# Performance work log

Hardware: AMD Instinct MI355X
Metric: run time of the kernel (lower is better)

The kernel has to match this reference:

```python
import jax, jax.numpy as jnp
import numpy as np

D = 384      # n_embed_dims
H = 6        # n_heads
HS = D // H  # head_size = 64
T = 256      # block_size
B = 256
EPS = 1e-5


def setup_inputs() -> dict:
    key = jax.random.key(0)
    ks = jax.random.split(key, 12)
    s_in = 1.0 / np.sqrt(D)
    s_ff = 1.0 / np.sqrt(4 * D)
    return {
        "x": jax.random.normal(ks[0], (B, T, D), jnp.float32),
        # per-head QKV weights, stacked [H, D, HS] (Linear bias=False)
        "wq": jax.random.normal(ks[1], (H, D, HS), jnp.float32) * s_in,
        "wk": jax.random.normal(ks[2], (H, D, HS), jnp.float32) * s_in,
        "wv": jax.random.normal(ks[3], (H, D, HS), jnp.float32) * s_in,
        "w_proj": jax.random.normal(ks[4], (D, D), jnp.float32) * s_in,
        "b_proj": jax.random.normal(ks[5], (D,), jnp.float32) * s_in,
        "w1": jax.random.normal(ks[6], (D, 4 * D), jnp.float32) * s_in,
        "b1": jax.random.normal(ks[7], (4 * D,), jnp.float32) * s_in,
        "w2": jax.random.normal(ks[8], (4 * D, D), jnp.float32) * s_ff,
        "b2": jax.random.normal(ks[9], (D,), jnp.float32) * s_ff,
        "g1": jnp.ones((D,), jnp.float32),
        "be1": jnp.zeros((D,), jnp.float32),
        "g2": jnp.ones((D,), jnp.float32),
        "be2": jnp.zeros((D,), jnp.float32),
    }


def _layernorm(x, g, b):
    mu = jnp.mean(x, axis=-1, keepdims=True)
    var = jnp.mean(jnp.square(x - mu), axis=-1, keepdims=True)
    return (x - mu) * jax.lax.rsqrt(var + EPS) * g + b


def _attention(x, wq, wk, wv, w_proj, b_proj):
    # faithful quirk: scale = 1/sqrt(C) with C = full embed dim (384)
    scale = 1.0 / jnp.sqrt(jnp.asarray(D, x.dtype))
    q = jnp.einsum("btd,hde->bhte", x, wq)  # [B,H,T,HS]
    k = jnp.einsum("btd,hde->bhte", x, wk)
    v = jnp.einsum("btd,hde->bhte", x, wv)
    w = jnp.einsum("bhte,bhse->bhts", q, k) * scale  # [B,H,T,T], no mask
    w = jax.nn.softmax(w, axis=-1)
    out = jnp.einsum("bhts,bhse->bhte", w, v)  # [B,H,T,HS]
    # concat heads along feature dim (head order matches torch cat)
    out = out.transpose(0, 2, 1, 3).reshape(x.shape[0], x.shape[1], D)
    return out @ w_proj + b_proj


def reference(x, wq, wk, wv, w_proj, b_proj, w1, b1, w2, b2, g1, be1, g2, be2):
    x = x + _attention(_layernorm(x, g1, be1), wq, wk, wv, w_proj, b_proj)
    h = _layernorm(x, g2, be2)
    h = jax.nn.relu(h @ w1 + b1) @ w2 + b2  # dropout = eval-mode identity
    return x + h
```

## Files before the change

### kernel.cpp

```cpp
#include <hip/hip_runtime.h>
#include <stdint.h>

#define NTOK 65536
#define DE 384
#define S_HEAD 25165824

typedef __bf16 bf16x8 __attribute__((ext_vector_type(8)));
typedef float  f32x4 __attribute__((ext_vector_type(4)));

__device__ __forceinline__ unsigned short f2bf(float f) {
  union { float fl; unsigned u; } a; a.fl = f;
  unsigned r = a.u + 0x7fffu + ((a.u >> 16) & 1u);
  return (unsigned short)(r >> 16);
}

__device__ __forceinline__ void gll16(const void* g, void* l) {
  __builtin_amdgcn_global_load_lds((const __attribute__((address_space(1))) void*)g,
                                   (__attribute__((address_space(3))) void*)l, 16, 0, 0);
}

__device__ __forceinline__ bf16x8 ds128(unsigned addr) {
  bf16x8 r;
  asm volatile("ds_read_b128 %0, %1" : "=v"(r) : "v"(addr));
  return r;
}

__global__ void pack_t(unsigned short* __restrict__ dst, const float* __restrict__ src,
                       int R, int C) {
  int t = blockIdx.x * 256 + threadIdx.x;
  if (t >= R * C) return;
  int r = t / C, c = t - r * C;
  dst[(size_t)c * R + r] = f2bf(src[t]);
}

__global__ void qkv_pack(const float* __restrict__ wq, const float* __restrict__ wk,
                         const float* __restrict__ wv, unsigned short* __restrict__ dst) {
  int t = blockIdx.x * 256 + threadIdx.x;
  if (t >= 3 * 147456) return;
  int which = t / 147456, r = t - which * 147456;
  const float* src = which == 0 ? wq : (which == 1 ? wk : wv);
  int h = r / 24576, r2 = r - h * 24576;
  int d = r2 >> 6, e = r2 & 63;
  dst[(size_t)(which * 384 + h * 64 + e) * 384 + d] = f2bf(src[r]);
}

__global__ __launch_bounds__(256) void ln_kernel(const float* __restrict__ x,
                                                 const float* __restrict__ g,
                                                 const float* __restrict__ be,
                                                 unsigned short* __restrict__ out) {
  int wave = threadIdx.x >> 6, lane = threadIdx.x & 63;
  size_t row = (size_t)blockIdx.x * 4 + wave;
  const float* xr = x + row * DE;
  int c0 = lane * 2;
  float2 v0 = *(const float2*)(xr + c0);
  float2 v1 = *(const float2*)(xr + 128 + c0);
  float2 v2 = *(const float2*)(xr + 256 + c0);
  float s  = v0.x + v0.y + v1.x + v1.y + v2.x + v2.y;
  float ss = v0.x*v0.x + v0.y*v0.y + v1.x*v1.x + v1.y*v1.y + v2.x*v2.x + v2.y*v2.y;
#pragma unroll
  for (int m = 1; m < 64; m <<= 1) { s += __shfl_xor(s, m); ss += __shfl_xor(ss, m); }
  float mu = s * (1.0f / 384.0f);
  float rstd = rsqrtf(ss * (1.0f / 384.0f) - mu * mu + 1e-5f);
  unsigned short* orow = out + row * DE;
  {
    float a0 = (v0.x - mu) * rstd * g[c0] + be[c0];
    float a1 = (v0.y - mu) * rstd * g[c0 + 1] + be[c0 + 1];
    *(unsigned*)(orow + c0) = (unsigned)f2bf(a0) | ((unsigned)f2bf(a1) << 16);
  }
  {
    int c = c0 + 128;
    float a0 = (v1.x - mu) * rstd * g[c] + be[c];
    float a1 = (v1.y - mu) * rstd * g[c + 1] + be[c + 1];
    *(unsigned*)(orow + c) = (unsigned)f2bf(a0) | ((unsigned)f2bf(a1) << 16);
  }
  {
    int c = c0 + 256;
    float a0 = (v2.x - mu) * rstd * g[c] + be[c];
    float a1 = (v2.y - mu) * rstd * g[c + 1] + be[c + 1];
    *(unsigned*)(orow + c) = (unsigned)f2bf(a0) | ((unsigned)f2bf(a1) << 16);
  }
}

template<int EPI>
__device__ __forceinline__
void gemm_core(const unsigned short* __restrict__ A, const unsigned short* __restrict__ Bt,
               int M, int N, int K, int ntx,
               const float* __restrict__ bias, const float* __restrict__ resid,
               float* __restrict__ outf, unsigned short* __restrict__ outb) {
  __shared__ __align__(16) unsigned short As[2][8192];
  __shared__ __align__(16) unsigned short Bs[2][8192];
  const int tid = threadIdx.x;
  const int wave = tid >> 6, lane = tid & 63;

  const int nwg = gridDim.x;
  const int cpx = nwg >> 3;
  const int wg = (blockIdx.x & 7) * cpx + (blockIdx.x >> 3);
  const int bx = wg % ntx, by = wg / ntx;
  const int mBase = by << 7, nBase = bx << 7;
  const int wm = (wave >> 1) << 6, wn = (wave & 1) << 6;
  const int fr = lane & 15, fg = lane >> 4;

  const unsigned asb = (unsigned)(uintptr_t)&As[0][0];
  const unsigned bsb = (unsigned)(uintptr_t)&Bs[0][0];

  f32x4 acc[4][4];
  const f32x4 z = {0.f, 0.f, 0.f, 0.f};
#pragma unroll
  for (int i = 0; i < 4; ++i)
#pragma unroll
    for (int j = 0; j < 4; ++j) acc[i][j] = z;

  auto stage = [&](int buf, int kt) {
#pragma unroll
    for (int i = 0; i < 4; ++i) {
      int Lb = i * 4096 + wave * 1024;
      int L = Lb + lane * 16;
      int row = L >> 7;
      int col = (((L >> 4) & 7) ^ (row & 7)) << 3;
      gll16(A + (size_t)(mBase + row) * K + kt + col, (unsigned short*)As[buf] + (Lb >> 1));
    }
#pragma unroll
    for (int i = 0; i < 4; ++i) {
      int Lb = i * 4096 + wave * 1024;
      int L = Lb + lane * 16;
      int row = L >> 7;
      int col = (((L >> 4) & 7) ^ (row & 7)) << 3;
      gll16(Bt + (size_t)(nBase + row) * K + kt + col, (unsigned short*)Bs[buf] + (Lb >> 1));
    }
  };

  const int NK = K >> 6;
  stage(0, 0);
  for (int t = 0; t < NK; ++t) {
    const int cur = t & 1;
    if (t + 1 < NK) {
      stage(cur ^ 1, (t + 1) << 6);
      asm volatile("s_waitcnt vmcnt(8)" ::: "memory");
    } else {
      asm volatile("s_waitcnt vmcnt(0)" ::: "memory");
    }
    asm volatile("" ::: "memory");
    __builtin_amdgcn_s_barrier();
    asm volatile("" ::: "memory");

    const unsigned ab = asb + (cur ? 16384u : 0u);
    const unsigned bb = bsb + (cur ? 16384u : 0u);
    bf16x8 af[2][4], bfr[2][4];
#pragma unroll
    for (int ks = 0; ks < 2; ++ks) {
#pragma unroll
      for (int mb = 0; mb < 4; ++mb) {
        int row = wm + mb * 16 + fr;
        unsigned byte = (unsigned)(row << 7) + ((unsigned)((ks * 4 + fg) ^ (row & 7)) << 4);
        af[ks][mb] = ds128(ab + byte);
      }
#pragma unroll
      for (int nb = 0; nb < 4; ++nb) {
        int row = wn + nb * 16 + fr;
        unsigned byte = (unsigned)(row << 7) + ((unsigned)((ks * 4 + fg) ^ (row & 7)) << 4);
        bfr[ks][nb] = ds128(bb + byte);
      }
    }
    asm volatile("s_waitcnt lgkmcnt(0)" ::: "memory");
    __builtin_amdgcn_sched_barrier(0);
    __builtin_amdgcn_s_setprio(1);
#pragma unroll
    for (int ks = 0; ks < 2; ++ks)
#pragma unroll
      for (int mb = 0; mb < 4; ++mb)
#pragma unroll
        for (int nb = 0; nb < 4; ++nb)
          acc[mb][nb] = __builtin_amdgcn_mfma_f32_16x16x32_bf16(af[ks][mb], bfr[ks][nb], acc[mb][nb], 0, 0, 0);
    __builtin_amdgcn_s_setprio(0);
    asm volatile("" ::: "memory");
    __builtin_amdgcn_s_barrier();
    asm volatile("" ::: "memory");
  }

#pragma unroll
  for (int mb = 0; mb < 4; ++mb) {
#pragma unroll
    for (int nb = 0; nb < 4; ++nb) {
      const int gn = nBase + wn + nb * 16 + fr;
#pragma unroll
      for (int i = 0; i < 4; ++i) {
        const int gm = mBase + wm + mb * 16 + (fg << 2) + i;
        float val = acc[mb][nb][i];
        if (EPI == 0) {
          int which = gn / 384;
          int rest = gn - which * 384;
          int hh = rest >> 6, e = rest & 63;
          int b = gm >> 8, tt = gm & 255;
          size_t idx;
          if (which < 2)
            idx = (size_t)which * S_HEAD + (((size_t)(b * 6 + hh) * 256 + tt) << 6) + e;
          else
            idx = 2 * (size_t)S_HEAD + (((size_t)(b * 6 + hh) * 64 + e) << 8) + tt;
          outb[idx] = f2bf(val);
        } else if (EPI == 1) {
          size_t idx = (size_t)gm * N + gn;
          outf[idx] = val + bias[gn] + resid[idx];
        } else if (EPI == 2) {
          float r = val + bias[gn];
          outb[(size_t)gm * N + gn] = f2bf(r > 0.f ? r : 0.f);
        } else {
          size_t idx = (size_t)gm * N + gn;
          outf[idx] = val + bias[gn] + resid[idx];
        }
      }
    }
  }
}

__global__ __launch_bounds__(256, 2)
void gemm_qkv(const unsigned short* __restrict__ A, const unsigned short* __restrict__ Bt,
              int M, int N, int K, int ntx, const float* __restrict__ bias,
              const float* __restrict__ resid, float* __restrict__ outf,
              unsigned short* __restrict__ outb) {
  gemm_core<0>(A, Bt, M, N, K, ntx, bias, resid, outf, outb);
}
__global__ __launch_bounds__(256, 2)
void gemm_proj(const unsigned short* __restrict__ A, const unsigned short* __restrict__ Bt,
               int M, int N, int K, int ntx, const float* __restrict__ bias,
               const float* __restrict__ resid, float* __restrict__ outf,
               unsigned short* __restrict__ outb) {
  gemm_core<1>(A, Bt, M, N, K, ntx, bias, resid, outf, outb);
}
__global__ __launch_bounds__(256, 2)
void gemm_mlp1(const unsigned short* __restrict__ A, const unsigned short* __restrict__ Bt,
               int M, int N, int K, int ntx, const float* __restrict__ bias,
               const float* __restrict__ resid, float* __restrict__ outf,
               unsigned short* __restrict__ outb) {
  gemm_core<2>(A, Bt, M, N, K, ntx, bias, resid, outf, outb);
}
__global__ __launch_bounds__(256, 2)
void gemm_mlp2(const unsigned short* __restrict__ A, const unsigned short* __restrict__ Bt,
               int M, int N, int K, int ntx, const float* __restrict__ bias,
               const float* __restrict__ resid, float* __restrict__ outf,
               unsigned short* __restrict__ outb) {
  gemm_core<3>(A, Bt, M, N, K, ntx, bias, resid, outf, outb);
}

__global__ __launch_bounds__(256)
void attn_kernel(const unsigned short* __restrict__ q, const unsigned short* __restrict__ kk,
                 const unsigned short* __restrict__ vt, unsigned short* __restrict__ o) {
  __shared__ unsigned short Pw[4][64 * 32];
  const int bh = blockIdx.x;
  const int b = bh / 6, h = bh - b * 6;
  const unsigned short* qb = q + (size_t)bh * 256 * 64;
  const unsigned short* kb = kk + (size_t)bh * 256 * 64;
  const unsigned short* vb = vt + (size_t)bh * 64 * 256;
  const int wave = threadIdx.x >> 6, lane = threadIdx.x & 63;
  const int fr = lane & 15, fg = lane >> 4;
  const int fk = fg << 3;
  const int qrow0 = wave << 6;
  const float scale = 0.051031036307982884f;
  const f32x4 z = {0.f, 0.f, 0.f, 0.f};

  bf16x8 qf[4][2];
#pragma unroll
  for (int rb = 0; rb < 4; ++rb)
#pragma unroll
    for (int ks = 0; ks < 2; ++ks)
      qf[rb][ks] = *(const bf16x8*)(qb + (qrow0 + rb * 16 + fr) * 64 + ks * 32 + fk);

  float pm[4][4];
#pragma unroll
  for (int rb = 0; rb < 4; ++rb)
#pragma unroll
    for (int i = 0; i < 4; ++i) pm[rb][i] = -1e30f;

  for (int cb = 0; cb < 16; ++cb) {
    bf16x8 kf0 = *(const bf16x8*)(kb + (cb * 16 + fr) * 64 + fk);
    bf16x8 kf1 = *(const bf16x8*)(kb + (cb * 16 + fr) * 64 + 32 + fk);
#pragma unroll
    for (int rb = 0; rb < 4; ++rb) {
      f32x4 s = __builtin_amdgcn_mfma_f32_16x16x32_bf16(qf[rb][0], kf0, z, 0, 0, 0);
      s = __builtin_amdgcn_mfma_f32_16x16x32_bf16(qf[rb][1], kf1, s, 0, 0, 0);
#pragma unroll
      for (int i = 0; i < 4; ++i) pm[rb][i] = fmaxf(pm[rb][i], s[i]);
    }
  }
#pragma unroll
  for (int rb = 0; rb < 4; ++rb)
#pragma unroll
    for (int i = 0; i < 4; ++i) {
      float v = pm[rb][i];
      v = fmaxf(v, __shfl_xor(v, 1));
      v = fmaxf(v, __shfl_xor(v, 2));
      v = fmaxf(v, __shfl_xor(v, 4));
      v = fmaxf(v, __shfl_xor(v, 8));
      pm[rb][i] = v;
    }

  f32x4 oacc[4][4];
  float psum[4][4];
#pragma unroll
  for (int rb = 0; rb < 4; ++rb)
#pragma unroll
    for (int nb = 0; nb < 4; ++nb) oacc[rb][nb] = z;
#pragma unroll
  for (int rb = 0; rb < 4; ++rb)
#pragma unroll
    for (int i = 0; i < 4; ++i) psum[rb][i] = 0.f;

  for (int kb2 = 0; kb2 < 8; ++kb2) {
#pragma unroll
    for (int c2 = 0; c2 < 2; ++c2) {
      int cb = kb2 * 2 + c2;
      bf16x8 kf0 = *(const bf16x8*)(kb + (cb * 16 + fr) * 64 + fk);
      bf16x8 kf1 = *(const bf16x8*)(kb + (cb * 16 + fr) * 64 + 32 + fk);
#pragma unroll
      for (int rb = 0; rb < 4; ++rb) {
        f32x4 s = __builtin_amdgcn_mfma_f32_16x16x32_bf16(qf[rb][0], kf0, z, 0, 0, 0);
        s = __builtin_amdgcn_mfma_f32_16x16x32_bf16(qf[rb][1], kf1, s, 0, 0, 0);
#pragma unroll
        for (int i = 0; i < 4; ++i) {
          float p = __expf(scale * (s[i] - pm[rb][i]));
          psum[rb][i] += p;
          Pw[wave][(rb * 16 + (fg << 2) + i) * 32 + c2 * 16 + fr] = f2bf(p);
        }
      }
    }
    bf16x8 pa[4], vf[4];
#pragma unroll
    for (int rb = 0; rb < 4; ++rb) pa[rb] = *(const bf16x8*)(&Pw[wave][(rb * 16 + fr) * 32 + fk]);
#pragma unroll
    for (int nb = 0; nb < 4; ++nb)
      vf[nb] = *(const bf16x8*)(vb + (nb * 16 + fr) * 256 + kb2 * 32 + fk);
#pragma unroll
    for (int rb = 0; rb < 4; ++rb)
#pragma unroll
      for (int nb = 0; nb < 4; ++nb)
        oacc[rb][nb] = __builtin_amdgcn_mfma_f32_16x16x32_bf16(pa[rb], vf[nb], oacc[rb][nb], 0, 0, 0);
  }

  float rs[4][4];
#pragma unroll
  for (int rb = 0; rb < 4; ++rb)
#pragma unroll
    for (int i = 0; i < 4; ++i) {
      float v = psum[rb][i];
      v += __shfl_xor(v, 1);
      v += __shfl_xor(v, 2);
      v += __shfl_xor(v, 4);
      v += __shfl_xor(v, 8);
      rs[rb][i] = 1.0f / v;
    }

#pragma unroll
  for (int rb = 0; rb < 4; ++rb)
#pragma unroll
    for (int nb = 0; nb < 4; ++nb)
#pragma unroll
      for (int i = 0; i < 4; ++i) {
        int token = b * 256 + qrow0 + rb * 16 + (fg << 2) + i;
        int gcol = h * 64 + nb * 16 + fr;
        o[(size_t)token * DE + gcol] = f2bf(oacc[rb][nb][i] * rs[rb][i]);
      }
}

extern "C" void kernel_launch(void* const* d_in, const int* in_sizes, int n_in,
                              void* d_out, int out_size, void* d_ws, size_t ws_size,
                              hipStream_t stream) {
  const float* x     = (const float*)d_in[0];
  const float* wq    = (const float*)d_in[1];
  const float* wk    = (const float*)d_in[2];
  const float* wv    = (const float*)d_in[3];
  const float* wproj = (const float*)d_in[4];
  const float* bproj = (const float*)d_in[5];
  const float* w1    = (const float*)d_in[6];
  const float* b1    = (const float*)d_in[7];
  const float* w2    = (const float*)d_in[8];
  const float* b2    = (const float*)d_in[9];
  const float* g1    = (const float*)d_in[10];
  const float* be1   = (const float*)d_in[11];
  const float* g2    = (const float*)d_in[12];
  const float* be2   = (const float*)d_in[13];

  char* ws = (char*)d_ws;
  unsigned short* xln   = (unsigned short*)(ws + 0);
  unsigned short* hbuf  = xln;
  unsigned short* qkv   = (unsigned short*)(ws + 50331648);
  unsigned short* attno = (unsigned short*)(ws + 201326592);
  unsigned short* act   = (unsigned short*)(ws + 50331648);
  float*          x1    = (float*)(ws + 251658240);
  unsigned short* wqkvt = (unsigned short*)(ws + 352321536);
  unsigned short* wprjt = (unsigned short*)(ws + 352321536 + 884736);
  unsigned short* w1t   = (unsigned short*)(ws + 352321536 + 884736 + 294912);
  unsigned short* w2t   = (unsigned short*)(ws + 352321536 + 884736 + 294912 + 1179648);

  qkv_pack<<<(3 * 147456 + 255) / 256, 256, 0, stream>>>(wq, wk, wv, wqkvt);
  pack_t<<<(147456 + 255) / 256, 256, 0, stream>>>(wprjt, wproj, 384, 384);
  pack_t<<<(589824 + 255) / 256, 256, 0, stream>>>(w1t, w1, 384, 1536);
  pack_t<<<(589824 + 255) / 256, 256, 0, stream>>>(w2t, w2, 1536, 384);

  ln_kernel<<<NTOK / 4, 256, 0, stream>>>(x, g1, be1, xln);

  gemm_qkv<<<512 * 9, 256, 0, stream>>>(xln, wqkvt, NTOK, 1152, 384, 9,
                                        nullptr, nullptr, nullptr, qkv);

  attn_kernel<<<1536, 256, 0, stream>>>(qkv, qkv + S_HEAD, qkv + 2 * (size_t)S_HEAD, attno);

  gemm_proj<<<512 * 3, 256, 0, stream>>>(attno, wprjt, NTOK, 384, 384, 3,
                                         bproj, x, x1, nullptr);

  ln_kernel<<<NTOK / 4, 256, 0, stream>>>(x1, g2, be2, hbuf);

  gemm_mlp1<<<512 * 12, 256, 0, stream>>>(hbuf, w1t, NTOK, 1536, 384, 12,
                                          b1, nullptr, nullptr, act);

  gemm_mlp2<<<512 * 3, 256, 0, stream>>>(act, w2t, NTOK, 384, 1536, 3,
                                         b2, x1, (float*)d_out, nullptr);
}
```

Baseline: 584.0 us.

## Use 256-wide GEMM tiles with 8 waves and row-major QKV output

Generalizes the GEMM core to templated block and wave tiling and moves all GEMMs to 256x256 or 256x128 tiles with 512 threads, loading A fragments in halves to limit register pressure. The QKV weight matrix is padded to 1280 columns so the QKV GEMM writes a plain row-major [tokens,1280] buffer instead of scattering per-head and transposed V. The attention kernel now reads Q/K with the wider stride and transposes V into swizzled shared memory itself. The intent is more operand reuse per tile and coalesced epilogue stores, at the cost of padding work, an extra LDS transpose in attention, and lower occupancy.

```diff
diff --git a/kernel.cpp b/kernel.cpp
--- a/kernel.cpp
+++ b/kernel.cpp
@@ -3,10 +3,11 @@
 
 #define NTOK 65536
 #define DE 384
-#define S_HEAD 25165824
+#define QSTR 1280
 
 typedef __bf16 bf16x8 __attribute__((ext_vector_type(8)));
 typedef float  f32x4 __attribute__((ext_vector_type(4)));
+typedef unsigned short u16x8 __attribute__((ext_vector_type(8)));
 
 __device__ __forceinline__ unsigned short f2bf(float f) {
   union { float fl; unsigned u; } a; a.fl = f;
@@ -36,12 +37,16 @@
 __global__ void qkv_pack(const float* __restrict__ wq, const float* __restrict__ wk,
                          const float* __restrict__ wv, unsigned short* __restrict__ dst) {
   int t = blockIdx.x * 256 + threadIdx.x;
-  if (t >= 3 * 147456) return;
-  int which = t / 147456, r = t - which * 147456;
-  const float* src = which == 0 ? wq : (which == 1 ? wk : wv);
-  int h = r / 24576, r2 = r - h * 24576;
-  int d = r2 >> 6, e = r2 & 63;
-  dst[(size_t)(which * 384 + h * 64 + e) * 384 + d] = f2bf(src[r]);
+  if (t >= QSTR * 384) return;
+  int n = t / 384, k = t - n * 384;
+  unsigned short v = 0;
+  if (n < 1152) {
+    int which = n / 384, r = n - which * 384;
+    const float* src = which == 0 ? wq : (which == 1 ? wk : wv);
+    int h = r >> 6, e = r & 63;
+    v = f2bf(src[h * 24576 + k * 64 + e]);
+  }
+  dst[t] = v;
 }
 
 __global__ __launch_bounds__(256) void ln_kernel(const float* __restrict__ x,
@@ -81,14 +86,20 @@
   }
 }
 
-template<int EPI>
+template<int EPI, int BM, int BN, int WM, int WN>
 __device__ __forceinline__
 void gemm_core(const unsigned short* __restrict__ A, const unsigned short* __restrict__ Bt,
                int M, int N, int K, int ntx,
                const float* __restrict__ bias, const float* __restrict__ resid,
                float* __restrict__ outf, unsigned short* __restrict__ outb) {
-  __shared__ __align__(16) unsigned short As[2][8192];
-  __shared__ __align__(16) unsigned short Bs[2][8192];
+  constexpr int T = WM * WN * 64;
+  constexpr int MWT = BM / WM, NWT = BN / WN;
+  constexpr int MF = MWT / 16, NF = NWT / 16;
+  constexpr int MH = MF / 4;
+  constexpr int LA = (BM * 128) / (T * 16);
+  constexpr int LB = (BN * 128) / (T * 16);
+  __shared__ __align__(16) unsigned short As[2][BM * 64];
+  __shared__ __align__(16) unsigned short Bs[2][BN * 64];
   const int tid = threadIdx.x;
   const int wave = tid >> 6, lane = tid & 63;
 
@@ -96,32 +107,33 @@
   const int cpx = nwg >> 3;
   const int wg = (blockIdx.x & 7) * cpx + (blockIdx.x >> 3);
   const int bx = wg % ntx, by = wg / ntx;
-  const int mBase = by << 7, nBase = bx << 7;
-  const int wm = (wave >> 1) << 6, wn = (wave & 1) << 6;
+  const int mBase = by * BM, nBase = bx * BN;
+  const int wmi = wave / WN, wni = wave % WN;
+  const int wm = wmi * MWT, wn = wni * NWT;
   const int fr = lane & 15, fg = lane >> 4;
 
   const unsigned asb = (unsigned)(uintptr_t)&As[0][0];
   const unsigned bsb = (unsigned)(uintptr_t)&Bs[0][0];
 
-  f32x4 acc[4][4];
+  f32x4 acc[MF][NF];
   const f32x4 z = {0.f, 0.f, 0.f, 0.f};
 #pragma unroll
-  for (int i = 0; i < 4; ++i)
-#pragma unroll
-    for (int j = 0; j < 4; ++j) acc[i][j] = z;
+  for (int i = 0; i < MF; ++i)
+#pragma unroll
+    for (int j = 0; j < NF; ++j) acc[i][j] = z;
 
   auto stage = [&](int buf, int kt) {
 #pragma unroll
-    for (int i = 0; i < 4; ++i) {
-      int Lb = i * 4096 + wave * 1024;
+    for (int i = 0; i < LA; ++i) {
+      int Lb = i * (T * 16) + wave * 1024;
       int L = Lb + lane * 16;
       int row = L >> 7;
       int col = (((L >> 4) & 7) ^ (row & 7)) << 3;
       gll16(A + (size_t)(mBase + row) * K + kt + col, (unsigned short*)As[buf] + (Lb >> 1));
     }
 #pragma unroll
-    for (int i = 0; i < 4; ++i) {
-      int Lb = i * 4096 + wave * 1024;
+    for (int i = 0; i < LB; ++i) {
+      int Lb = i * (T * 16) + wave * 1024;
       int L = Lb + lane * 16;
       int row = L >> 7;
       int col = (((L >> 4) & 7) ^ (row & 7)) << 3;
@@ -135,7 +147,8 @@
     const int cur = t & 1;
     if (t + 1 < NK) {
       stage(cur ^ 1, (t + 1) << 6);
-      asm volatile("s_waitcnt vmcnt(8)" ::: "memory");
+      if constexpr (LA + LB == 8) asm volatile("s_waitcnt vmcnt(8)" ::: "memory");
+      else                        asm volatile("s_waitcnt vmcnt(6)" ::: "memory");
     } else {
       asm volatile("s_waitcnt vmcnt(0)" ::: "memory");
     }
@@ -143,60 +156,54 @@
     __builtin_amdgcn_s_barrier();
     asm volatile("" ::: "memory");
 
-    const unsigned ab = asb + (cur ? 16384u : 0u);
-    const unsigned bb = bsb + (cur ? 16384u : 0u);
-    bf16x8 af[2][4], bfr[2][4];
+    const unsigned ab = asb + (cur ? (unsigned)(BM * 128) : 0u);
+    const unsigned bb = bsb + (cur ? (unsigned)(BN * 128) : 0u);
 #pragma unroll
     for (int ks = 0; ks < 2; ++ks) {
-#pragma unroll
-      for (int mb = 0; mb < 4; ++mb) {
-        int row = wm + mb * 16 + fr;
-        unsigned byte = (unsigned)(row << 7) + ((unsigned)((ks * 4 + fg) ^ (row & 7)) << 4);
-        af[ks][mb] = ds128(ab + byte);
-      }
-#pragma unroll
-      for (int nb = 0; nb < 4; ++nb) {
+      bf16x8 bfr[NF];
+#pragma unroll
+      for (int nb = 0; nb < NF; ++nb) {
         int row = wn + nb * 16 + fr;
         unsigned byte = (unsigned)(row << 7) + ((unsigned)((ks * 4 + fg) ^ (row & 7)) << 4);
-        bfr[ks][nb] = ds128(bb + byte);
+        bfr[nb] = ds128(bb + byte);
       }
-    }
-    asm volatile("s_waitcnt lgkmcnt(0)" ::: "memory");
-    __builtin_amdgcn_sched_barrier(0);
-    __builtin_amdgcn_s_setprio(1);
-#pragma unroll
-    for (int ks = 0; ks < 2; ++ks)
-#pragma unroll
-      for (int mb = 0; mb < 4; ++mb)
-#pragma unroll
-        for (int nb = 0; nb < 4; ++nb)
-          acc[mb][nb] = __builtin_amdgcn_mfma_f32_16x16x32_bf16(af[ks][mb], bfr[ks][nb], acc[mb][nb], 0, 0, 0);
-    __builtin_amdgcn_s_setprio(0);
+#pragma unroll
+      for (int mh = 0; mh < MH; ++mh) {
+        bf16x8 af[4];
+#pragma unroll
+        for (int mb = 0; mb < 4; ++mb) {
+          int row = wm + (mh * 4 + mb) * 16 + fr;
+          unsigned byte = (unsigned)(row << 7) + ((unsigned)((ks * 4 + fg) ^ (row & 7)) << 4);
+          af[mb] = ds128(ab + byte);
+        }
+        asm volatile("s_waitcnt lgkmcnt(0)" ::: "memory");
+        __builtin_amdgcn_sched_barrier(0);
+        __builtin_amdgcn_s_setprio(1);
+#pragma unroll
+        for (int mb = 0; mb < 4; ++mb)
+#pragma unroll
+          for (int nb = 0; nb < NF; ++nb)
+            acc[mh * 4 + mb][nb] =
+                __builtin_amdgcn_mfma_f32_16x16x32_bf16(af[mb], bfr[nb], acc[mh * 4 + mb][nb], 0, 0, 0);
+        __builtin_amdgcn_s_setprio(0);
+      }
+    }
     asm volatile("" ::: "memory");
     __builtin_amdgcn_s_barrier();
     asm volatile("" ::: "memory");
   }
 
 #pragma unroll
-  for (int mb = 0; mb < 4; ++mb) {
-#pragma unroll
-    for (int nb = 0; nb < 4; ++nb) {
+  for (int mb = 0; mb < MF; ++mb) {
+#pragma unroll
+    for (int nb = 0; nb < NF; ++nb) {
       const int gn = nBase + wn + nb * 16 + fr;
 #pragma unroll
       for (int i = 0; i < 4; ++i) {
         const int gm = mBase + wm + mb * 16 + (fg << 2) + i;
         float val = acc[mb][nb][i];
         if (EPI == 0) {
-          int which = gn / 384;
-          int rest = gn - which * 384;
-          int hh = rest >> 6, e = rest & 63;
-          int b = gm >> 8, tt = gm & 255;
-          size_t idx;
-          if (which < 2)
-            idx = (size_t)which * S_HEAD + (((size_t)(b * 6 + hh) * 256 + tt) << 6) + e;
-          else
-            idx = 2 * (size_t)S_HEAD + (((size_t)(b * 6 + hh) * 64 + e) << 8) + tt;
-          outb[idx] = f2bf(val);
+          outb[(size_t)gm * N + gn] = f2bf(val);
         } else if (EPI == 1) {
           size_t idx = (size_t)gm * N + gn;
           outf[idx] = val + bias[gn] + resid[idx];
@@ -212,44 +219,45 @@
   }
 }
 
-__global__ __launch_bounds__(256, 2)
+__global__ __launch_bounds__(512, 1)
 void gemm_qkv(const unsigned short* __restrict__ A, const unsigned short* __restrict__ Bt,
               int M, int N, int K, int ntx, const float* __restrict__ bias,
               const float* __restrict__ resid, float* __restrict__ outf,
               unsigned short* __restrict__ outb) {
-  gemm_core<0>(A, Bt, M, N, K, ntx, bias, resid, outf, outb);
-}
-__global__ __launch_bounds__(256, 2)
+  gemm_core<0, 256, 256, 2, 4>(A, Bt, M, N, K, ntx, bias, resid, outf, outb);
+}
+__global__ __launch_bounds__(512, 1)
 void gemm_proj(const unsigned short* __restrict__ A, const unsigned short* __restrict__ Bt,
                int M, int N, int K, int ntx, const float* __restrict__ bias,
                const float* __restrict__ resid, float* __restrict__ outf,
                unsigned short* __restrict__ outb) {
-  gemm_core<1>(A, Bt, M, N, K, ntx, bias, resid, outf, outb);
-}
-__global__ __launch_bounds__(256, 2)
+  gemm_core<1, 256, 128, 4, 2>(A, Bt, M, N, K, ntx, bias, resid, outf, outb);
+}
+__global__ __launch_bounds__(512, 1)
 void gemm_mlp1(const unsigned short* __restrict__ A, const unsigned short* __restrict__ Bt,
                int M, int N, int K, int ntx, const float* __restrict__ bias,
                const float* __restrict__ resid, float* __restrict__ outf,
                unsigned short* __restrict__ outb) {
-  gemm_core<2>(A, Bt, M, N, K, ntx, bias, resid, outf, outb);
-}
-__global__ __launch_bounds__(256, 2)
+  gemm_core<2, 256, 256, 2, 4>(A, Bt, M, N, K, ntx, bias, resid, outf, outb);
+}
+__global__ __launch_bounds__(512, 1)
 void gemm_mlp2(const unsigned short* __restrict__ A, const unsigned short* __restrict__ Bt,
                int M, int N, int K, int ntx, const float* __restrict__ bias,
                const float* __restrict__ resid, float* __restrict__ outf,
                unsigned short* __restrict__ outb) {
-  gemm_core<3>(A, Bt, M, N, K, ntx, bias, resid, outf, outb);
+  gemm_core<3, 256, 128, 4, 2>(A, Bt, M, N, K, ntx, bias, resid, outf, outb);
 }
 
 __global__ __launch_bounds__(256)
-void attn_kernel(const unsigned short* __restrict__ q, const unsigned short* __restrict__ kk,
-                 const unsigned short* __restrict__ vt, unsigned short* __restrict__ o) {
+void attn_kernel(const unsigned short* __restrict__ qkvn, unsigned short* __restrict__ o) {
+  __shared__ unsigned short Vt[64 * 256];
   __shared__ unsigned short Pw[4][64 * 32];
   const int bh = blockIdx.x;
   const int b = bh / 6, h = bh - b * 6;
-  const unsigned short* qb = q + (size_t)bh * 256 * 64;
-  const unsigned short* kb = kk + (size_t)bh * 256 * 64;
-  const unsigned short* vb = vt + (size_t)bh * 64 * 256;
+  const unsigned short* base = qkvn + (size_t)(b * 256) * QSTR;
+  const unsigned short* qb = base + h * 64;
+  const unsigned short* kbp = base + 384 + h * 64;
+  const unsigned short* vbp = base + 768 + h * 64;
   const int wave = threadIdx.x >> 6, lane = threadIdx.x & 63;
   const int fr = lane & 15, fg = lane >> 4;
   const int fk = fg << 3;
@@ -257,12 +265,24 @@
   const float scale = 0.051031036307982884f;
   const f32x4 z = {0.f, 0.f, 0.f, 0.f};
 
+  {
+    const int s = threadIdx.x;
+    u16x8 v8[8];
+#pragma unroll
+    for (int j = 0; j < 8; ++j)
+      v8[j] = *(const u16x8*)(vbp + (size_t)s * QSTR + j * 8);
+#pragma unroll
+    for (int e = 0; e < 64; ++e)
+      Vt[(e << 8) + (s ^ ((e & 7) << 3))] = v8[e >> 3][e & 7];
+  }
+  __syncthreads();
+
   bf16x8 qf[4][2];
 #pragma unroll
   for (int rb = 0; rb < 4; ++rb)
 #pragma unroll
     for (int ks = 0; ks < 2; ++ks)
-      qf[rb][ks] = *(const bf16x8*)(qb + (qrow0 + rb * 16 + fr) * 64 + ks * 32 + fk);
+      qf[rb][ks] = *(const bf16x8*)(qb + (size_t)(qrow0 + rb * 16 + fr) * QSTR + ks * 32 + fk);
 
   float pm[4][4];
 #pragma unroll
@@ -271,8 +291,8 @@
     for (int i = 0; i < 4; ++i) pm[rb][i] = -1e30f;
 
   for (int cb = 0; cb < 16; ++cb) {
-    bf16x8 kf0 = *(const bf16x8*)(kb + (cb * 16 + fr) * 64 + fk);
-    bf16x8 kf1 = *(const bf16x8*)(kb + (cb * 16 + fr) * 64 + 32 + fk);
+    bf16x8 kf0 = *(const bf16x8*)(kbp + (size_t)(cb * 16 + fr) * QSTR + fk);
+    bf16x8 kf1 = *(const bf16x8*)(kbp + (size_t)(cb * 16 + fr) * QSTR + 32 + fk);
 #pragma unroll
     for (int rb = 0; rb < 4; ++rb) {
       f32x4 s = __builtin_amdgcn_mfma_f32_16x16x32_bf16(qf[rb][0], kf0, z, 0, 0, 0);
@@ -308,8 +328,8 @@
 #pragma unroll
     for (int c2 = 0; c2 < 2; ++c2) {
       int cb = kb2 * 2 + c2;
-      bf16x8 kf0 = *(const bf16x8*)(kb + (cb * 16 + fr) * 64 + fk);
-      bf16x8 kf1 = *(const bf16x8*)(kb + (cb * 16 + fr) * 64 + 32 + fk);
+      bf16x8 kf0 = *(const bf16x8*)(kbp + (size_t)(cb * 16 + fr) * QSTR + fk);
+      bf16x8 kf1 = *(const bf16x8*)(kbp + (size_t)(cb * 16 + fr) * QSTR + 32 + fk);
 #pragma unroll
       for (int rb = 0; rb < 4; ++rb) {
         f32x4 s = __builtin_amdgcn_mfma_f32_16x16x32_bf16(qf[rb][0], kf0, z, 0, 0, 0);
@@ -326,8 +346,10 @@
 #pragma unroll
     for (int rb = 0; rb < 4; ++rb) pa[rb] = *(const bf16x8*)(&Pw[wave][(rb * 16 + fr) * 32 + fk]);
 #pragma unroll
-    for (int nb = 0; nb < 4; ++nb)
-      vf[nb] = *(const bf16x8*)(vb + (nb * 16 + fr) * 256 + kb2 * 32 + fk);
+    for (int nb = 0; nb < 4; ++nb) {
+      int e = nb * 16 + fr;
+      vf[nb] = *(const bf16x8*)(&Vt[(e << 8) + ((kb2 * 32 + fk) ^ ((e & 7) << 3))]);
+    }
 #pragma unroll
     for (int rb = 0; rb < 4; ++rb)
 #pragma unroll
@@ -380,36 +402,36 @@
 
   char* ws = (char*)d_ws;
   unsigned short* xln   = (unsigned short*)(ws + 0);
-  unsigned short* hbuf  = xln;
-  unsigned short* qkv   = (unsigned short*)(ws + 50331648);
-  unsigned short* attno = (unsigned short*)(ws + 201326592);
-  unsigned short* act   = (unsigned short*)(ws + 50331648);
-  float*          x1    = (float*)(ws + 251658240);
+  float*          x1    = (float*)(ws + 0);
+  unsigned short* qkvn  = (unsigned short*)(ws + 50331648);
+  unsigned short* hbuf  = (unsigned short*)(ws + 100663296);
+  unsigned short* act   = (unsigned short*)(ws + 150994944);
+  unsigned short* attno = (unsigned short*)(ws + 218103808);
   unsigned short* wqkvt = (unsigned short*)(ws + 352321536);
-  unsigned short* wprjt = (unsigned short*)(ws + 352321536 + 884736);
-  unsigned short* w1t   = (unsigned short*)(ws + 352321536 + 884736 + 294912);
-  unsigned short* w2t   = (unsigned short*)(ws + 352321536 + 884736 + 294912 + 1179648);
-
-  qkv_pack<<<(3 * 147456 + 255) / 256, 256, 0, stream>>>(wq, wk, wv, wqkvt);
+  unsigned short* wprjt = (unsigned short*)(ws + 352321536 + 983040);
+  unsigned short* w1t   = (unsigned short*)(ws + 352321536 + 983040 + 294912);
+  unsigned short* w2t   = (unsigned short*)(ws + 352321536 + 983040 + 294912 + 1179648);
+
+  qkv_pack<<<(QSTR * 384 + 255) / 256, 256, 0, stream>>>(wq, wk, wv, wqkvt);
   pack_t<<<(147456 + 255) / 256, 256, 0, stream>>>(wprjt, wproj, 384, 384);
   pack_t<<<(589824 + 255) / 256, 256, 0, stream>>>(w1t, w1, 384, 1536);
   pack_t<<<(589824 + 255) / 256, 256, 0, stream>>>(w2t, w2, 1536, 384);
 
   ln_kernel<<<NTOK / 4, 256, 0, stream>>>(x, g1, be1, xln);
 
-  gemm_qkv<<<512 * 9, 256, 0, stream>>>(xln, wqkvt, NTOK, 1152, 384, 9,
-                                        nullptr, nullptr, nullptr, qkv);
-
-  attn_kernel<<<1536, 256, 0, stream>>>(qkv, qkv + S_HEAD, qkv + 2 * (size_t)S_HEAD, attno);
-
-  gemm_proj<<<512 * 3, 256, 0, stream>>>(attno, wprjt, NTOK, 384, 384, 3,
+  gemm_qkv<<<5 * 256, 512, 0, stream>>>(xln, wqkvt, NTOK, QSTR, 384, 5,
+                                        nullptr, nullptr, nullptr, qkvn);
+
+  attn_kernel<<<1536, 256, 0, stream>>>(qkvn, attno);
+
+  gemm_proj<<<3 * 256, 512, 0, stream>>>(attno, wprjt, NTOK, 384, 384, 3,
                                          bproj, x, x1, nullptr);
 
   ln_kernel<<<NTOK / 4, 256, 0, stream>>>(x1, g2, be2, hbuf);
 
-  gemm_mlp1<<<512 * 12, 256, 0, stream>>>(hbuf, w1t, NTOK, 1536, 384, 12,
-                                          b1, nullptr, nullptr, act);
-
-  gemm_mlp2<<<512 * 3, 256, 0, stream>>>(act, w2t, NTOK, 384, 1536, 3,
+  gemm_mlp1<<<6 * 256, 512, 0, stream>>>(hbuf, w1t, NTOK, 1536, 384, 6,
+                                         b1, nullptr, nullptr, act);
+
+  gemm_mlp2<<<3 * 256, 512, 0, stream>>>(act, w2t, NTOK, 384, 1536, 3,
                                          b2, x1, (float*)d_out, nullptr);
 }
```

Result: faster. 559.1 us (-4.3%).
